# Kernel tuning notes

Hardware: AMD Instinct MI355X
Metric: run time of the kernel (lower is better)

## Reference

```python
import jax, jax.numpy as jnp
import numpy as np

B, S, F, RANK = 8, 4096, 1024, 64


def gram_schmidt(P):
    """Sequential Gram-Schmidt on columns of P (F, R) -> orthogonal (unnormalized) columns.
    Matches vizbert's orth_tensor: v_i = p_i - sum_{j<i} ((u_j . v)/(u_j . u_j)) u_j.
    Each step vectorizes the inner projection loop as one matmul (u_j are mutually
    orthogonal, so sequential-update and batched coefficients are equal in exact math)."""
    us = [P[:, 0]]
    for i in range(1, P.shape[1]):
        U = jnp.stack(us, axis=1)                 # (F, i)
        sq = jnp.sum(U * U, axis=0)               # (i,)
        v = P[:, i]
        coeff = (U.T @ v) / sq                    # (i,)
        us.append(v - U @ coeff)
    return jnp.stack(us, axis=1)                  # (F, R)


def setup_inputs() -> dict:
    key = jax.random.key(0)
    k1, k2 = jax.random.split(key)
    hidden_states = jax.random.normal(k1, (B, S, F), dtype=jnp.float32)
    # probe params initialized uniform(-0.05, 0.05), stacked to (num_features, rank)
    probe = jax.random.uniform(k2, (F, RANK), minval=-0.05, maxval=0.05, dtype=jnp.float32)
    return {"hidden_states": hidden_states, "probe": probe}


def reference(hidden_states, probe):
    # orth_probe: Gram-Schmidt orthogonalized probe columns (orthogonalize=True)
    U = gram_schmidt(probe)                       # (F, R), orthogonal columns
    sq = jnp.sum(U * U, axis=0)                   # (R,) squared norms

    # normalize=True: remember per-token norms before projection
    old_norms = jnp.linalg.norm(hidden_states, axis=2, keepdims=True)  # (B, S, 1)
    # mask_first=True: remember first-token states
    first_state = hidden_states[:, 0]             # (B, F)

    # full_batch_gs: subtract projection onto each probe direction.
    # Because U's columns are orthogonal, the sequential per-column subtraction
    # equals one fused projection: h - U (U^T h / ||u||^2).
    coeffs = jnp.einsum('bsf,fr->bsr', hidden_states, U) / sq
    h = hidden_states - jnp.einsum('bsr,fr->bsf', coeffs, U)

    # normalize=True: rescale back to the original per-token norm
    new_norms = jnp.linalg.norm(h, axis=2, keepdims=True)
    h = h / new_norms * old_norms

    # mask_first=True: restore the first token untouched
    h = h.at[:, 0].set(first_state)
    return h
```

## Files before the change

### kernel.cpp

```cpp
#include <hip/hip_runtime.h>


typedef __attribute__((ext_vector_type(8))) short bf16x8;
typedef __attribute__((ext_vector_type(4))) float f32x4;

#define MFMA_B16(a, b, c) __builtin_amdgcn_mfma_f32_16x16x32_bf16((a), (b), (c), 0, 0, 0)

__device__ __forceinline__ unsigned short bf16bits(float x) {
  union { float f; unsigned u; } v; v.f = x;
  return (unsigned short)((v.u + 0x7fffu + ((v.u >> 16) & 1u)) >> 16);
}
__device__ __forceinline__ unsigned pack2(float a, float b) {
  return (unsigned)bf16bits(a) | ((unsigned)bf16bits(b) << 16);
}
__device__ __forceinline__ bf16x8 cvt8(const float* p) {
  f32x4 v0 = *(const f32x4*)p;
  f32x4 v1 = *(const f32x4*)(p + 4);
  bf16x8 r;
  r[0] = (short)bf16bits(v0[0]); r[1] = (short)bf16bits(v0[1]);
  r[2] = (short)bf16bits(v0[2]); r[3] = (short)bf16bits(v0[3]);
  r[4] = (short)bf16bits(v1[0]); r[5] = (short)bf16bits(v1[1]);
  r[6] = (short)bf16bits(v1[2]); r[7] = (short)bf16bits(v1[3]);
  return r;
}

__global__ void pp_gram(const float* __restrict__ P, float* __restrict__ partial) {
  __shared__ float Pl[64][68];
  const int tid = threadIdx.x, ch = blockIdx.x;
  #pragma unroll
  for (int u = 0; u < 4; ++u) {
    const int f = tid >> 2, r = (tid & 3) * 16 + 4 * u;
    *(f32x4*)&Pl[f][r] = *(const f32x4*)(P + (size_t)(ch * 64 + f) * 64 + r);
  }
  __syncthreads();
  const int a0 = (tid >> 4) * 4, b0 = (tid & 15) * 4;
  f32x4 acc[4];
  #pragma unroll
  for (int i = 0; i < 4; ++i) acc[i] = (f32x4){0.f, 0.f, 0.f, 0.f};
  for (int k = 0; k < 64; ++k) {
    f32x4 av = *(const f32x4*)&Pl[k][a0];
    f32x4 bv = *(const f32x4*)&Pl[k][b0];
    #pragma unroll
    for (int i = 0; i < 4; ++i) acc[i] += av[i] * bv;
  }
  #pragma unroll
  for (int i = 0; i < 4; ++i)
    *(f32x4*)(partial + (size_t)ch * 4096 + (size_t)(a0 + i) * 64 + b0) = acc[i];
}

__global__ void pp_invert(const float* __restrict__ partial, float* __restrict__ W) {
  __shared__ float A[64][68];
  const int tid = threadIdx.x;
  const int i = tid >> 2, q = tid & 3, q16 = (tid & 3) * 16;
  #pragma unroll
  for (int u = 0; u < 4; ++u) {
    f32x4 s = (f32x4){0.f, 0.f, 0.f, 0.f};
    const int off = i * 64 + q16 + 4 * u;
    for (int p = 0; p < 16; ++p) s += *(const f32x4*)(partial + (size_t)p * 4096 + off);
    *(f32x4*)&A[i][q16 + 4 * u] = s;
  }
  __syncthreads();
  for (int k = 0; k < 64; ++k) {
    const float d = 1.0f / A[k][k];
    const float f = A[i][k];
    f32x4 prs[4], cur[4];
    #pragma unroll
    for (int u = 0; u < 4; ++u) {
      prs[u] = *(const f32x4*)&A[k][q16 + 4 * u];
      cur[u] = *(const f32x4*)&A[i][q16 + 4 * u];
    }
    __syncthreads();
    const int kl = k - q16;
    #pragma unroll
    for (int u = 0; u < 4; ++u) {
      f32x4 pv = prs[u] * d;
      if (kl >= u * 4 && kl < u * 4 + 4) { pv[kl - u * 4] = d; cur[u][kl - u * 4] = 0.f; }
      f32x4 res = (i == k) ? pv : (cur[u] - f * pv);
      *(f32x4*)&A[i][q16 + 4 * u] = res;
    }
    __syncthreads();
  }
  #pragma unroll
  for (int u = 0; u < 4; ++u)
    *(f32x4*)(W + (size_t)i * 64 + q16 + 4 * u) = *(const f32x4*)&A[i][q16 + 4 * u];
}

__global__ void pp_pack(const float* __restrict__ P, unsigned short* __restrict__ Ptb,
                        unsigned short* __restrict__ Pb) {
  const int g = blockIdx.x * 256 + threadIdx.x;
  const int flat = g * 4;
  const int f = flat >> 6, r = flat & 63;
  f32x4 v = *(const f32x4*)(P + flat);
  unsigned short b[4];
  #pragma unroll
  for (int u = 0; u < 4; ++u) b[u] = bf16bits(v[u]);
  unsigned lo = (unsigned)b[0] | ((unsigned)b[1] << 16);
  unsigned hi = (unsigned)b[2] | ((unsigned)b[3] << 16);
  *(unsigned long long*)(Pb + flat) = (unsigned long long)lo | ((unsigned long long)hi << 32);
  #pragma unroll
  for (int u = 0; u < 4; ++u) Ptb[(size_t)(r + u) * 1024 + f] = b[u];
}

__global__ __launch_bounds__(256, 2) void pp_main(
    const float* __restrict__ H, const unsigned short* __restrict__ Ptb,
    const unsigned short* __restrict__ Pb, const float* __restrict__ W,
    float* __restrict__ out) {
  __shared__ unsigned short Ha[64][136];
  __shared__ float Yl[64][68];
  __shared__ float Cl[64][68];
  __shared__ unsigned short Wl[64][72];
  __shared__ float rowsq[64], dotv[64], scalev[64];

  const int tid = threadIdx.x;
  const int lane = tid & 63, wid = tid >> 6;
  const int c16 = lane & 15, quad = lane >> 4;
  const int strip = wid * 16;
  const int srow = tid >> 2, sg = tid & 3;
  const long row0 = (long)blockIdx.x * 64;

  if (tid < 64) { rowsq[tid] = 0.f; dotv[tid] = 0.f; }
  for (int u = tid; u < 4096; u += 256) Wl[u >> 6][u & 63] = bf16bits(W[u]);

  f32x4 accY[4];
  #pragma unroll
  for (int t = 0; t < 4; ++t) accY[t] = (f32x4){0.f, 0.f, 0.f, 0.f};

  float sqacc = 0.f;
  const float* hrow = H + (row0 + srow) * 1024 + sg * 32;

  for (int ch = 0; ch < 8; ++ch) {
    const float* hp = hrow + ch * 128;
    #pragma unroll
    for (int u = 0; u < 8; ++u) {
      f32x4 v = *(const f32x4*)(hp + 4 * u);
      sqacc += v[0] * v[0] + v[1] * v[1] + v[2] * v[2] + v[3] * v[3];
      unsigned lo = pack2(v[0], v[1]), hi = pack2(v[2], v[3]);
      *(unsigned long long*)&Ha[srow][sg * 32 + 4 * u] =
          (unsigned long long)lo | ((unsigned long long)hi << 32);
    }
    __syncthreads();
    #pragma unroll
    for (int it = 0; it < 4; ++it) {
      bf16x8 a = *(const bf16x8*)&Ha[strip + c16][it * 32 + quad * 8];
      const unsigned short* bp = Ptb + (size_t)c16 * 1024 + ch * 128 + it * 32 + quad * 8;
      #pragma unroll
      for (int t = 0; t < 4; ++t) {
        bf16x8 b = *(const bf16x8*)(bp + (size_t)t * 16 * 1024);
        accY[t] = MFMA_B16(a, b, accY[t]);
      }
    }
    __syncthreads();
  }
  atomicAdd(&rowsq[srow], sqacc);
  #pragma unroll
  for (int t = 0; t < 4; ++t)
    #pragma unroll
    for (int r = 0; r < 4; ++r)
      Yl[strip + quad * 4 + r][t * 16 + c16] = accY[t][r];
  __syncthreads();

  f32x4 accC[4];
  #pragma unroll
  for (int t = 0; t < 4; ++t) accC[t] = (f32x4){0.f, 0.f, 0.f, 0.f};
  #pragma unroll
  for (int kk = 0; kk < 2; ++kk) {
    bf16x8 a = cvt8(&Yl[strip + c16][kk * 32 + quad * 8]);
    #pragma unroll
    for (int t = 0; t < 4; ++t) {
      bf16x8 b = *(const bf16x8*)&Wl[t * 16 + c16][kk * 32 + quad * 8];
      accC[t] = MFMA_B16(a, b, accC[t]);
    }
  }
  #pragma unroll
  for (int t = 0; t < 4; ++t)
    #pragma unroll
    for (int r = 0; r < 4; ++r) Cl[strip + quad * 4 + r][t * 16 + c16] = accC[t][r];
  __syncthreads();

  {
    float d = 0.f;
    #pragma unroll
    for (int u = 0; u < 4; ++u) {
      f32x4 yv = *(const f32x4*)&Yl[srow][sg * 16 + 4 * u];
      f32x4 cv = *(const f32x4*)&Cl[srow][sg * 16 + 4 * u];
      d += yv[0] * cv[0] + yv[1] * cv[1] + yv[2] * cv[2] + yv[3] * cv[3];
    }
    atomicAdd(&dotv[srow], d);
  }
  __syncthreads();
  if (tid < 64) {
    float o2 = rowsq[tid];
    float n2 = fmaxf(o2 - dotv[tid], 1e-30f);
    scalev[tid] = sqrtf(o2 / n2);
  }
  __syncthreads();

  bf16x8 ca0 = cvt8(&Cl[strip + c16][quad * 8]);
  bf16x8 ca1 = cvt8(&Cl[strip + c16][32 + quad * 8]);
  float sc[4]; long rg[4]; bool fs[4];
  #pragma unroll
  for (int r = 0; r < 4; ++r) {
    const int m = strip + quad * 4 + r;
    sc[r] = scalev[m];
    rg[r] = row0 + m;
    fs[r] = ((rg[r] & 4095) == 0);
  }
  for (int ft = 0; ft < 64; ++ft) {
    const unsigned short* bp = Pb + (size_t)(ft * 16 + c16) * 64 + quad * 8;
    bf16x8 b0 = *(const bf16x8*)bp;
    bf16x8 b1 = *(const bf16x8*)(bp + 32);
    f32x4 acc = (f32x4){0.f, 0.f, 0.f, 0.f};
    acc = MFMA_B16(ca0, b0, acc);
    acc = MFMA_B16(ca1, b1, acc);
    const int f = ft * 16 + c16;
    #pragma unroll
    for (int r = 0; r < 4; ++r) {
      const long idx = rg[r] * 1024 + f;
      const float h = H[idx];
      out[idx] = fs[r] ? h : (h - acc[r]) * sc[r];
    }
  }
}

extern "C" void kernel_launch(void* const* d_in, const int* in_sizes, int n_in,
                              void* d_out, int out_size, void* d_ws, size_t ws_size,
                              hipStream_t stream) {
  const float* H = (const float*)d_in[0];
  const float* P = (const float*)d_in[1];
  float* out = (float*)d_out;
  float* ws = (float*)d_ws;
  float* W = ws;
  float* partial = ws + 4096;
  unsigned short* Ptb = (unsigned short*)(ws + 4096 + 16 * 4096);
  unsigned short* Pb = Ptb + 65536;

  pp_gram<<<16, 256, 0, stream>>>(P, partial);
  pp_invert<<<1, 256, 0, stream>>>(partial, W);
  pp_pack<<<64, 256, 0, stream>>>(P, Ptb, Pb);
  pp_main<<<512, 256, 0, stream>>>(H, Ptb, Pb, W, out);
}
```

Before: 325.4 us.

## Fuse prep kernels, drop LDS staging of H, use per-wave reductions

Merges the Gram and bf16 packing kernels into one prep kernel and has the inverse kernel emit bf16 weights directly, removing a launch and a conversion pass. The main kernel loads H straight into MFMA A-fragments from global memory instead of staging it through LDS, computes norms and dot products with wave shuffles instead of shared atomics, and raises launch bounds to four blocks per CU. Output writes become nontemporal stores. The A-fragment loads from H are now strided per lane (16 rows by 32 bytes per quad), which may hurt coalescing compared with the previous row-contiguous loads.

```diff
diff --git a/kernel.cpp b/kernel.cpp
--- a/kernel.cpp
+++ b/kernel.cpp
@@ -1,4 +1,5 @@
 #include <hip/hip_runtime.h>
+#include <hip/hip_bf16.h>
 
 
 typedef __attribute__((ext_vector_type(8))) short bf16x8;
@@ -10,21 +11,22 @@
   union { float f; unsigned u; } v; v.f = x;
   return (unsigned short)((v.u + 0x7fffu + ((v.u >> 16) & 1u)) >> 16);
 }
-__device__ __forceinline__ unsigned pack2(float a, float b) {
-  return (unsigned)bf16bits(a) | ((unsigned)bf16bits(b) << 16);
-}
+
+__device__ __forceinline__ bf16x8 packbf8(f32x4 v0, f32x4 v1) {
+  union { bf16x8 v; __hip_bfloat162 h[4]; } u;
+  u.h[0] = __float22bfloat162_rn(make_float2(v0[0], v0[1]));
+  u.h[1] = __float22bfloat162_rn(make_float2(v0[2], v0[3]));
+  u.h[2] = __float22bfloat162_rn(make_float2(v1[0], v1[1]));
+  u.h[3] = __float22bfloat162_rn(make_float2(v1[2], v1[3]));
+  return u.v;
+}
+
 __device__ __forceinline__ bf16x8 cvt8(const float* p) {
-  f32x4 v0 = *(const f32x4*)p;
-  f32x4 v1 = *(const f32x4*)(p + 4);
-  bf16x8 r;
-  r[0] = (short)bf16bits(v0[0]); r[1] = (short)bf16bits(v0[1]);
-  r[2] = (short)bf16bits(v0[2]); r[3] = (short)bf16bits(v0[3]);
-  r[4] = (short)bf16bits(v1[0]); r[5] = (short)bf16bits(v1[1]);
-  r[6] = (short)bf16bits(v1[2]); r[7] = (short)bf16bits(v1[3]);
-  return r;
-}
-
-__global__ void pp_gram(const float* __restrict__ P, float* __restrict__ partial) {
+  return packbf8(*(const f32x4*)p, *(const f32x4*)(p + 4));
+}
+
+__global__ void pp_prep(const float* __restrict__ P, float* __restrict__ partial,
+                        unsigned short* __restrict__ Ptb, unsigned short* __restrict__ Pb) {
   __shared__ float Pl[64][68];
   const int tid = threadIdx.x, ch = blockIdx.x;
   #pragma unroll
@@ -46,12 +48,27 @@
   #pragma unroll
   for (int i = 0; i < 4; ++i)
     *(f32x4*)(partial + (size_t)ch * 4096 + (size_t)(a0 + i) * 64 + b0) = acc[i];
-}
-
-__global__ void pp_invert(const float* __restrict__ partial, float* __restrict__ W) {
+  const int f = tid >> 2, c0 = (tid & 3) * 16;
+  const int gf = ch * 64 + f;
+  unsigned short b16[16];
+  #pragma unroll
+  for (int u = 0; u < 16; ++u) b16[u] = bf16bits(Pl[f][c0 + u]);
+  #pragma unroll
+  for (int u = 0; u < 16; ++u) Ptb[(size_t)(c0 + u) * 1024 + gf] = b16[u];
+  #pragma unroll
+  for (int w = 0; w < 4; ++w) {
+    unsigned long long q = (unsigned long long)b16[4 * w] |
+                           ((unsigned long long)b16[4 * w + 1] << 16) |
+                           ((unsigned long long)b16[4 * w + 2] << 32) |
+                           ((unsigned long long)b16[4 * w + 3] << 48);
+    *(unsigned long long*)(Pb + (size_t)gf * 64 + c0 + 4 * w) = q;
+  }
+}
+
+__global__ void pp_invert(const float* __restrict__ partial, unsigned short* __restrict__ Wb) {
   __shared__ float A[64][68];
   const int tid = threadIdx.x;
-  const int i = tid >> 2, q = tid & 3, q16 = (tid & 3) * 16;
+  const int i = tid >> 2, q16 = (tid & 3) * 16;
   #pragma unroll
   for (int u = 0; u < 4; ++u) {
     f32x4 s = (f32x4){0.f, 0.f, 0.f, 0.f};
@@ -81,134 +98,96 @@
     __syncthreads();
   }
   #pragma unroll
-  for (int u = 0; u < 4; ++u)
-    *(f32x4*)(W + (size_t)i * 64 + q16 + 4 * u) = *(const f32x4*)&A[i][q16 + 4 * u];
-}
-
-__global__ void pp_pack(const float* __restrict__ P, unsigned short* __restrict__ Ptb,
-                        unsigned short* __restrict__ Pb) {
-  const int g = blockIdx.x * 256 + threadIdx.x;
-  const int flat = g * 4;
-  const int f = flat >> 6, r = flat & 63;
-  f32x4 v = *(const f32x4*)(P + flat);
-  unsigned short b[4];
-  #pragma unroll
-  for (int u = 0; u < 4; ++u) b[u] = bf16bits(v[u]);
-  unsigned lo = (unsigned)b[0] | ((unsigned)b[1] << 16);
-  unsigned hi = (unsigned)b[2] | ((unsigned)b[3] << 16);
-  *(unsigned long long*)(Pb + flat) = (unsigned long long)lo | ((unsigned long long)hi << 32);
-  #pragma unroll
-  for (int u = 0; u < 4; ++u) Ptb[(size_t)(r + u) * 1024 + f] = b[u];
-}
-
-__global__ __launch_bounds__(256, 2) void pp_main(
+  for (int u = 0; u < 4; ++u) {
+    #pragma unroll
+    for (int j = 0; j < 4; ++j) Wb[(size_t)i * 64 + q16 + 4 * u + j] = bf16bits(A[i][q16 + 4 * u + j]);
+  }
+}
+
+__global__ __launch_bounds__(256, 4) void pp_main(
     const float* __restrict__ H, const unsigned short* __restrict__ Ptb,
-    const unsigned short* __restrict__ Pb, const float* __restrict__ W,
+    const unsigned short* __restrict__ Pb, const unsigned short* __restrict__ Wb,
     float* __restrict__ out) {
-  __shared__ unsigned short Ha[64][136];
-  __shared__ float Yl[64][68];
-  __shared__ float Cl[64][68];
-  __shared__ unsigned short Wl[64][72];
-  __shared__ float rowsq[64], dotv[64], scalev[64];
-
-  const int tid = threadIdx.x;
-  const int lane = tid & 63, wid = tid >> 6;
+  __shared__ float Yl[4][16][68];
+  __shared__ float Cl[4][16][68];
+
+  const int tid = threadIdx.x, wid = tid >> 6, lane = tid & 63;
   const int c16 = lane & 15, quad = lane >> 4;
-  const int strip = wid * 16;
-  const int srow = tid >> 2, sg = tid & 3;
-  const long row0 = (long)blockIdx.x * 64;
-
-  if (tid < 64) { rowsq[tid] = 0.f; dotv[tid] = 0.f; }
-  for (int u = tid; u < 4096; u += 256) Wl[u >> 6][u & 63] = bf16bits(W[u]);
+  const long rowbase = (long)blockIdx.x * 64 + wid * 16;
+  const float* hrow = H + (rowbase + c16) * 1024 + quad * 8;
 
   f32x4 accY[4];
   #pragma unroll
   for (int t = 0; t < 4; ++t) accY[t] = (f32x4){0.f, 0.f, 0.f, 0.f};
-
-  float sqacc = 0.f;
-  const float* hrow = H + (row0 + srow) * 1024 + sg * 32;
-
-  for (int ch = 0; ch < 8; ++ch) {
-    const float* hp = hrow + ch * 128;
-    #pragma unroll
-    for (int u = 0; u < 8; ++u) {
-      f32x4 v = *(const f32x4*)(hp + 4 * u);
-      sqacc += v[0] * v[0] + v[1] * v[1] + v[2] * v[2] + v[3] * v[3];
-      unsigned lo = pack2(v[0], v[1]), hi = pack2(v[2], v[3]);
-      *(unsigned long long*)&Ha[srow][sg * 32 + 4 * u] =
-          (unsigned long long)lo | ((unsigned long long)hi << 32);
-    }
-    __syncthreads();
-    #pragma unroll
-    for (int it = 0; it < 4; ++it) {
-      bf16x8 a = *(const bf16x8*)&Ha[strip + c16][it * 32 + quad * 8];
-      const unsigned short* bp = Ptb + (size_t)c16 * 1024 + ch * 128 + it * 32 + quad * 8;
-      #pragma unroll
-      for (int t = 0; t < 4; ++t) {
-        bf16x8 b = *(const bf16x8*)(bp + (size_t)t * 16 * 1024);
-        accY[t] = MFMA_B16(a, b, accY[t]);
-      }
-    }
-    __syncthreads();
-  }
-  atomicAdd(&rowsq[srow], sqacc);
+  float sq = 0.f;
+  const unsigned short* pB = Ptb + (size_t)c16 * 1024 + quad * 8;
+  #pragma unroll 4
+  for (int kk = 0; kk < 32; ++kk) {
+    f32x4 v0 = *(const f32x4*)(hrow + kk * 32);
+    f32x4 v1 = *(const f32x4*)(hrow + kk * 32 + 4);
+    sq += v0[0] * v0[0] + v0[1] * v0[1] + v0[2] * v0[2] + v0[3] * v0[3];
+    sq += v1[0] * v1[0] + v1[1] * v1[1] + v1[2] * v1[2] + v1[3] * v1[3];
+    bf16x8 a = packbf8(v0, v1);
+    #pragma unroll
+    for (int t = 0; t < 4; ++t) {
+      bf16x8 b = *(const bf16x8*)(pB + (size_t)t * 16 * 1024 + kk * 32);
+      accY[t] = MFMA_B16(a, b, accY[t]);
+    }
+  }
+  sq += __shfl_xor(sq, 16, 64);
+  sq += __shfl_xor(sq, 32, 64);
   #pragma unroll
   for (int t = 0; t < 4; ++t)
     #pragma unroll
     for (int r = 0; r < 4; ++r)
-      Yl[strip + quad * 4 + r][t * 16 + c16] = accY[t][r];
-  __syncthreads();
-
+      Yl[wid][quad * 4 + r][t * 16 + c16] = accY[t][r];
+  __syncthreads();
+
+  bf16x8 ya0 = cvt8(&Yl[wid][c16][quad * 8]);
+  bf16x8 ya1 = cvt8(&Yl[wid][c16][32 + quad * 8]);
   f32x4 accC[4];
   #pragma unroll
   for (int t = 0; t < 4; ++t) accC[t] = (f32x4){0.f, 0.f, 0.f, 0.f};
-  #pragma unroll
-  for (int kk = 0; kk < 2; ++kk) {
-    bf16x8 a = cvt8(&Yl[strip + c16][kk * 32 + quad * 8]);
-    #pragma unroll
-    for (int t = 0; t < 4; ++t) {
-      bf16x8 b = *(const bf16x8*)&Wl[t * 16 + c16][kk * 32 + quad * 8];
-      accC[t] = MFMA_B16(a, b, accC[t]);
-    }
+  const unsigned short* wB = Wb + (size_t)c16 * 64 + quad * 8;
+  #pragma unroll
+  for (int t = 0; t < 4; ++t) {
+    bf16x8 b0 = *(const bf16x8*)(wB + (size_t)t * 16 * 64);
+    bf16x8 b1 = *(const bf16x8*)(wB + (size_t)t * 16 * 64 + 32);
+    accC[t] = MFMA_B16(ya0, b0, accC[t]);
+    accC[t] = MFMA_B16(ya1, b1, accC[t]);
   }
   #pragma unroll
   for (int t = 0; t < 4; ++t)
     #pragma unroll
-    for (int r = 0; r < 4; ++r) Cl[strip + quad * 4 + r][t * 16 + c16] = accC[t][r];
-  __syncthreads();
-
-  {
-    float d = 0.f;
-    #pragma unroll
-    for (int u = 0; u < 4; ++u) {
-      f32x4 yv = *(const f32x4*)&Yl[srow][sg * 16 + 4 * u];
-      f32x4 cv = *(const f32x4*)&Cl[srow][sg * 16 + 4 * u];
-      d += yv[0] * cv[0] + yv[1] * cv[1] + yv[2] * cv[2] + yv[3] * cv[3];
-    }
-    atomicAdd(&dotv[srow], d);
-  }
-  __syncthreads();
-  if (tid < 64) {
-    float o2 = rowsq[tid];
-    float n2 = fmaxf(o2 - dotv[tid], 1e-30f);
-    scalev[tid] = sqrtf(o2 / n2);
-  }
-  __syncthreads();
-
-  bf16x8 ca0 = cvt8(&Cl[strip + c16][quad * 8]);
-  bf16x8 ca1 = cvt8(&Cl[strip + c16][32 + quad * 8]);
+    for (int r = 0; r < 4; ++r) Cl[wid][quad * 4 + r][t * 16 + c16] = accC[t][r];
+  __syncthreads();
+
+  float d = 0.f;
+  #pragma unroll
+  for (int u = 0; u < 4; ++u) {
+    f32x4 yv = *(const f32x4*)&Yl[wid][c16][quad * 16 + 4 * u];
+    f32x4 cv = *(const f32x4*)&Cl[wid][c16][quad * 16 + 4 * u];
+    d += yv[0] * cv[0] + yv[1] * cv[1] + yv[2] * cv[2] + yv[3] * cv[3];
+  }
+  d += __shfl_xor(d, 16, 64);
+  d += __shfl_xor(d, 32, 64);
+  const float scl = sqrtf(sq / fmaxf(sq - d, 1e-30f));
+
+  bf16x8 ca0 = cvt8(&Cl[wid][c16][quad * 8]);
+  bf16x8 ca1 = cvt8(&Cl[wid][c16][32 + quad * 8]);
   float sc[4]; long rg[4]; bool fs[4];
   #pragma unroll
   for (int r = 0; r < 4; ++r) {
-    const int m = strip + quad * 4 + r;
-    sc[r] = scalev[m];
-    rg[r] = row0 + m;
+    const int m = quad * 4 + r;
+    sc[r] = __shfl(scl, m, 64);
+    rg[r] = rowbase + m;
     fs[r] = ((rg[r] & 4095) == 0);
   }
+  const unsigned short* pb3 = Pb + (size_t)c16 * 64 + quad * 8;
+  #pragma unroll 2
   for (int ft = 0; ft < 64; ++ft) {
-    const unsigned short* bp = Pb + (size_t)(ft * 16 + c16) * 64 + quad * 8;
-    bf16x8 b0 = *(const bf16x8*)bp;
-    bf16x8 b1 = *(const bf16x8*)(bp + 32);
+    bf16x8 b0 = *(const bf16x8*)(pb3 + (size_t)ft * 16 * 64);
+    bf16x8 b1 = *(const bf16x8*)(pb3 + (size_t)ft * 16 * 64 + 32);
     f32x4 acc = (f32x4){0.f, 0.f, 0.f, 0.f};
     acc = MFMA_B16(ca0, b0, acc);
     acc = MFMA_B16(ca1, b1, acc);
@@ -217,7 +196,8 @@
     for (int r = 0; r < 4; ++r) {
       const long idx = rg[r] * 1024 + f;
       const float h = H[idx];
-      out[idx] = fs[r] ? h : (h - acc[r]) * sc[r];
+      const float o = fs[r] ? h : (h - acc[r]) * sc[r];
+      __builtin_nontemporal_store(o, &out[idx]);
     }
   }
 }
@@ -229,13 +209,12 @@
   const float* P = (const float*)d_in[1];
   float* out = (float*)d_out;
   float* ws = (float*)d_ws;
-  float* W = ws;
-  float* partial = ws + 4096;
-  unsigned short* Ptb = (unsigned short*)(ws + 4096 + 16 * 4096);
+  float* partial = ws;
+  unsigned short* Ptb = (unsigned short*)(ws + 16 * 4096);
   unsigned short* Pb = Ptb + 65536;
-
-  pp_gram<<<16, 256, 0, stream>>>(P, partial);
-  pp_invert<<<1, 256, 0, stream>>>(partial, W);
-  pp_pack<<<64, 256, 0, stream>>>(P, Ptb, Pb);
-  pp_main<<<512, 256, 0, stream>>>(H, Ptb, Pb, W, out);
-}
+  unsigned short* Wb = Pb + 65536;
+
+  pp_prep<<<16, 256, 0, stream>>>(P, partial, Ptb, Pb);
+  pp_invert<<<1, 256, 0, stream>>>(partial, Wb);
+  pp_main<<<512, 256, 0, stream>>>(H, Ptb, Pb, Wb, out);
+}
```

Result: no change. 328.5 us (+0.9%).
